# Kernel tuning notes

Hardware: AMD Instinct MI355X
Metric: run time of the kernel (lower is better)

The kernel has to match this reference:

```python
import jax, jax.numpy as jnp
import numpy as np

B, C, H = 8, 768, 12
TH = TW = 16
SH = SW = 32
N = TH * TW + SH * SW  # 1280


def setup_inputs() -> dict:
    key = jax.random.key(0)
    k1, k2, k3 = jax.random.split(key, 3)
    return {
        "x": jax.random.normal(k1, (B, N, C), jnp.float32),
        "qkv_w": jax.random.normal(k2, (3 * C, C), jnp.float32) * 0.02,
        "proj_w": jax.random.normal(k3, (C, C), jnp.float32) * 0.02,
        "proj_b": jnp.zeros((C,), jnp.float32),
        "t_h": TH, "t_w": TW, "s_h": SH, "s_w": SW,
    }


def reference(x, qkv_w, proj_w, proj_b, t_h, t_w, s_h, s_w):
    Bb, Nn, Cc = x.shape
    hd = Cc // H
    scale = hd ** -0.5
    nt = t_h * t_w
    ns = s_h * s_w
    # qkv projection: torch Linear computes x @ W.T
    qkv = (x @ qkv_w.T).reshape(Bb, Nn, 3, H, hd).transpose(2, 0, 3, 1, 4)
    q, k, v = qkv[0], qkv[1], qkv[2]  # each [B, H, N, hd]
    q_mt, q_s = q[:, :, :nt], q[:, :, nt:]
    k_mt, v_mt = k[:, :, :nt], v[:, :, :nt]
    # template queries attend only to template keys
    attn_t = jax.nn.softmax(jnp.einsum('bhqd,bhkd->bhqk', q_mt, k_mt) * scale, axis=-1)
    x_mt = jnp.einsum('bhqk,bhkd->bhqd', attn_t, v_mt).transpose(0, 2, 1, 3).reshape(Bb, nt, Cc)
    # search queries attend to all (template + search) keys
    attn_s = jax.nn.softmax(jnp.einsum('bhqd,bhkd->bhqk', q_s, k) * scale, axis=-1)
    x_s = jnp.einsum('bhqk,bhkd->bhqd', attn_s, v).transpose(0, 2, 1, 3).reshape(Bb, ns, Cc)
    out = jnp.concatenate([x_mt, x_s], axis=1)
    out = out @ proj_w.T + proj_b
    return out
```

## Files before the change

kernel.cpp:

```cpp
#include <hip/hip_runtime.h>
#include <hip/hip_bf16.h>


typedef __attribute__((ext_vector_type(8))) short s8v;
typedef __attribute__((ext_vector_type(4))) float f4v;
typedef __attribute__((ext_vector_type(4))) unsigned short u4v;
typedef __attribute__((ext_vector_type(4))) unsigned int u4i;
typedef __attribute__((ext_vector_type(2))) unsigned int u2i;

#define MFMA16(a, b, c) __builtin_amdgcn_mfma_f32_16x16x32_bf16((a), (b), (c), 0, 0, 0)

#define QSCALE 0.1803368801f

__device__ __forceinline__ unsigned short f2bf(float f) {
  unsigned int u = __builtin_bit_cast(unsigned int, f);
  u += 0x7fffu + ((u >> 16) & 1u);
  return (unsigned short)(u >> 16);
}

__device__ __forceinline__ unsigned int pk2(float lo, float hi) {
  __hip_bfloat162 t = __float22bfloat162_rn(make_float2(lo, hi));
  unsigned int u;
  __builtin_memcpy(&u, &t, 4);
  return u;
}

__device__ __forceinline__ s8v pack8(const float* p0, const float* p1) {
  u4i pi;
  pi[0] = pk2(p0[0], p0[1]);
  pi[1] = pk2(p0[2], p0[3]);
  pi[2] = pk2(p1[0], p1[1]);
  pi[3] = pk2(p1[2], p1[3]);
  return __builtin_bit_cast(s8v, pi);
}

__global__ __launch_bounds__(256) void cvt3_kernel(const float* __restrict__ x,
                                                   const float* __restrict__ wq,
                                                   const float* __restrict__ wp,
                                                   unsigned short* __restrict__ xb,
                                                   unsigned short* __restrict__ wqb,
                                                   unsigned short* __restrict__ wpb) {
  int i = blockIdx.x * 256 + threadIdx.x;
  const float* src;
  unsigned short* dst;
  int j;
  if (i < 1966080) {
    src = x; dst = xb; j = i;
  } else if (i < 1966080 + 442368) {
    src = wq; dst = wqb; j = i - 1966080;
  } else {
    src = wp; dst = wpb; j = i - (1966080 + 442368);
  }
  f4v v = ((const f4v*)src)[j];
  u4v o;
  o[0] = f2bf(v[0]); o[1] = f2bf(v[1]); o[2] = f2bf(v[2]); o[3] = f2bf(v[3]);
  ((u4v*)dst)[j] = o;
}


#define GEMM_STAGE(AS, BS, kt_)                                                             \
  do {                                                                                      \
    __builtin_amdgcn_global_load_lds(                                                       \
        (const __attribute__((address_space(1))) unsigned int*)(gA0 + (kt_)),               \
        (__attribute__((address_space(3))) unsigned int*)((char*)(AS) + tid * 16), 16, 0, 0); \
    __builtin_amdgcn_global_load_lds(                                                       \
        (const __attribute__((address_space(1))) unsigned int*)(gB0 + (kt_)),               \
        (__attribute__((address_space(3))) unsigned int*)((char*)(BS) + tid * 16), 16, 0, 0); \
    __builtin_amdgcn_global_load_lds(                                                       \
        (const __attribute__((address_space(1))) unsigned int*)(gA1 + (kt_)),               \
        (__attribute__((address_space(3))) unsigned int*)((char*)(AS) + (256 + tid) * 16),  \
        16, 0, 0);                                                                          \
    __builtin_amdgcn_global_load_lds(                                                       \
        (const __attribute__((address_space(1))) unsigned int*)(gB1 + (kt_)),               \
        (__attribute__((address_space(3))) unsigned int*)((char*)(BS) + (256 + tid) * 16),  \
        16, 0, 0);                                                                          \
  } while (0)

#define PIPE_WAIT4(cond_more)                                                               \
  do {                                                                                      \
    if (cond_more) asm volatile("s_waitcnt vmcnt(4) lgkmcnt(0)" ::: "memory");              \
    else           asm volatile("s_waitcnt vmcnt(0) lgkmcnt(0)" ::: "memory");              \
    __builtin_amdgcn_s_barrier();                                                           \
    __builtin_amdgcn_sched_barrier(0);                                                      \
  } while (0)

__global__ __launch_bounds__(256) void gemm_qkv_kernel(
    const unsigned short* __restrict__ A,
    const unsigned short* __restrict__ Bm,
    unsigned short* __restrict__ qb, unsigned short* __restrict__ kb,
    unsigned short* __restrict__ vT) {
  const int K = 768;
  __shared__ __align__(16) unsigned short As[3][128 * 32];
  __shared__ __align__(16) unsigned short Bs[3][128 * 32];
  int tid = threadIdx.x;
  int wave = tid >> 6, lane = tid & 63;
  int quad = lane >> 4, l16 = lane & 15;
  int wm = wave >> 1, wn = wave & 1;
  int l = blockIdx.x;
  int xcd = l & 7;
  int idx = l >> 3;
  int by = xcd * 10 + idx / 18;
  int bxg = idx - (idx / 18) * 18;
  int m0 = by * 128, n0 = bxg * 128;

  int srow = tid >> 2;
  int scol = (((tid & 3) ^ ((tid >> 3) & 3)) << 3);
  const unsigned short* gA0 = A + (size_t)(m0 + srow) * K + scol;
  const unsigned short* gA1 = A + (size_t)(m0 + srow + 64) * K + scol;
  const unsigned short* gB0 = Bm + (size_t)(n0 + srow) * K + scol;
  const unsigned short* gB1 = Bm + (size_t)(n0 + srow + 64) * K + scol;

  int rquad = quad ^ ((l16 >> 1) & 3);

  f4v acc[4][4];
#pragma unroll
  for (int i = 0; i < 4; ++i)
#pragma unroll
    for (int j = 0; j < 4; ++j) acc[i][j] = (f4v){0.f, 0.f, 0.f, 0.f};

  GEMM_STAGE(As[0], Bs[0], 0);
  GEMM_STAGE(As[1], Bs[1], 32);

  int bfc = 0, bfs = 2;
  for (int t = 0; t < 24; ++t) {
    PIPE_WAIT4(t + 1 < 24);
    if (t + 2 < 24) GEMM_STAGE(As[bfs], Bs[bfs], (t + 2) * 32);

    const unsigned short* Ab = As[bfc];
    const unsigned short* Bb = Bs[bfc];
    s8v af[4], bfr[4];
#pragma unroll
    for (int mi = 0; mi < 4; ++mi)
      af[mi] = *(const s8v*)&Ab[(wm * 64 + mi * 16 + l16) * 32 + rquad * 8];
#pragma unroll
    for (int ni = 0; ni < 4; ++ni)
      bfr[ni] = *(const s8v*)&Bb[(wn * 64 + ni * 16 + l16) * 32 + rquad * 8];
#pragma unroll
    for (int mi = 0; mi < 4; ++mi)
#pragma unroll
      for (int ni = 0; ni < 4; ++ni)
        acc[mi][ni] = MFMA16(af[mi], bfr[ni], acc[mi][ni]);

    bfc = (bfc == 2) ? 0 : bfc + 1;
    bfs = (bfs == 2) ? 0 : bfs + 1;
  }

  int which = n0 / 768;
  if (which == 2) {
#pragma unroll
    for (int ni = 0; ni < 4; ++ni) {
      int oo = n0 + wn * 64 + ni * 16 + l16 - 1536;
      int hh = oo >> 6;
      int dd = oo & 63;
#pragma unroll
      for (int mi = 0; mi < 4; ++mi) {
        int gm = m0 + wm * 64 + mi * 16 + quad * 4;
        int bb = gm / 1280;
        int nn = gm - bb * 1280;
        u2i w;
        w[0] = pk2(acc[mi][ni][0], acc[mi][ni][1]);
        w[1] = pk2(acc[mi][ni][2], acc[mi][ni][3]);
        *(u2i*)(vT + (((size_t)bb * 12 + hh) * 64 + dd) * 1280 + nn) = w;
      }
    }
  } else {
    unsigned short* dst = which ? kb : qb;
    float sc = which ? 1.0f : QSCALE;
#pragma unroll
    for (int ni = 0; ni < 4; ++ni) {
      int oo = n0 + wn * 64 + ni * 16 + l16 - which * 768;
      int hh = oo >> 6;
      int dd = oo & 63;
#pragma unroll
      for (int mi = 0; mi < 4; ++mi) {
#pragma unroll
        for (int r = 0; r < 4; ++r) {
          int gm = m0 + wm * 64 + mi * 16 + quad * 4 + r;
          int bb = gm / 1280;
          int nn = gm - bb * 1280;
          dst[(((size_t)bb * 12 + hh) * 1280 + nn) * 64 + dd] = f2bf(acc[mi][ni][r] * sc);
        }
      }
    }
  }
}

__global__ __launch_bounds__(256) void gemm_proj_kernel(
    const unsigned short* __restrict__ A,
    const unsigned short* __restrict__ Bm,
    const float* __restrict__ pb, float* __restrict__ out) {
  const int K = 768;
  __shared__ __align__(16) unsigned short As[3][128 * 32];
  __shared__ __align__(16) unsigned short Bs[3][128 * 32];
  int tid = threadIdx.x;
  int wave = tid >> 6, lane = tid & 63;
  int quad = lane >> 4, l16 = lane & 15;
  int wm = wave >> 1, wn = wave & 1;
  int l = blockIdx.x;
  int xcd = l & 7;
  int idx = l >> 3;
  int by = xcd * 10 + idx / 6;
  int bxg = idx - (idx / 6) * 6;
  int m0 = by * 128, n0 = bxg * 128;

  int srow = tid >> 2;
  int scol = (((tid & 3) ^ ((tid >> 3) & 3)) << 3);
  const unsigned short* gA0 = A + (size_t)(m0 + srow) * K + scol;
  const unsigned short* gA1 = A + (size_t)(m0 + srow + 64) * K + scol;
  const unsigned short* gB0 = Bm + (size_t)(n0 + srow) * K + scol;
  const unsigned short* gB1 = Bm + (size_t)(n0 + srow + 64) * K + scol;

  int rquad = quad ^ ((l16 >> 1) & 3);

  f4v acc[4][4];
#pragma unroll
  for (int i = 0; i < 4; ++i)
#pragma unroll
    for (int j = 0; j < 4; ++j) acc[i][j] = (f4v){0.f, 0.f, 0.f, 0.f};

  GEMM_STAGE(As[0], Bs[0], 0);
  GEMM_STAGE(As[1], Bs[1], 32);

  int bfc = 0, bfs = 2;
  for (int t = 0; t < 24; ++t) {
    PIPE_WAIT4(t + 1 < 24);
    if (t + 2 < 24) GEMM_STAGE(As[bfs], Bs[bfs], (t + 2) * 32);

    const unsigned short* Ab = As[bfc];
    const unsigned short* Bb = Bs[bfc];
    s8v af[4], bfr[4];
#pragma unroll
    for (int mi = 0; mi < 4; ++mi)
      af[mi] = *(const s8v*)&Ab[(wm * 64 + mi * 16 + l16) * 32 + rquad * 8];
#pragma unroll
    for (int ni = 0; ni < 4; ++ni)
      bfr[ni] = *(const s8v*)&Bb[(wn * 64 + ni * 16 + l16) * 32 + rquad * 8];
#pragma unroll
    for (int mi = 0; mi < 4; ++mi)
#pragma unroll
      for (int ni = 0; ni < 4; ++ni)
        acc[mi][ni] = MFMA16(af[mi], bfr[ni], acc[mi][ni]);

    bfc = (bfc == 2) ? 0 : bfc + 1;
    bfs = (bfs == 2) ? 0 : bfs + 1;
  }

#pragma unroll
  for (int ni = 0; ni < 4; ++ni) {
    int gn = n0 + wn * 64 + ni * 16 + l16;
    float bias = pb[gn];
#pragma unroll
    for (int mi = 0; mi < 4; ++mi)
#pragma unroll
      for (int r = 0; r < 4; ++r) {
        int gm = m0 + wm * 64 + mi * 16 + quad * 4 + r;
        out[(size_t)gm * 768 + gn] = acc[mi][ni][r] + bias;
      }
  }
}

__global__ __launch_bounds__(256) void attn_kernel(
    const unsigned short* __restrict__ qb, const unsigned short* __restrict__ kb,
    const unsigned short* __restrict__ vT, unsigned short* __restrict__ attnb) {
  const int NT = 1280, CC = 768;
  int l = blockIdx.x;
  int xcd = l & 7;
  int idx = l >> 3;
  int grp = xcd * 12 + idx / 10;
  int bx = idx - (idx / 10) * 10;
  int b = grp / 12;
  int h = grp - b * 12;
  int nk, qstart;
  if (bx < 8) { nk = 1280; qstart = 256 + bx * 128; }
  else        { nk = 256;  qstart = (bx - 8) * 128; }
  int wave = threadIdx.x >> 6, lane = threadIdx.x & 63;
  int quad = lane >> 4, l16 = lane & 15;
  int qa = qstart + wave * 32;
  int ntiles = nk >> 6;

  const unsigned short* qp = qb + (((size_t)b * 12 + h) * NT + qa) * 64;
  const unsigned short* kp = kb + (((size_t)b * 12 + h) * NT) * 64;
  const unsigned short* vp = vT + (((size_t)b * 12 + h) * 64) * NT;

  __shared__ __align__(16) unsigned short Kl[3][8][512];
  __shared__ __align__(16) unsigned short Vl[3][8][512];

  s8v bq0 = *(const s8v*)(qp + l16 * 64 + quad * 8);
  s8v bq1 = *(const s8v*)(qp + l16 * 64 + 32 + quad * 8);
  s8v bq2 = *(const s8v*)(qp + (16 + l16) * 64 + quad * 8);
  s8v bq3 = *(const s8v*)(qp + (16 + l16) * 64 + 32 + quad * 8);

  int perm = ((l16 >> 2) << 3) + (l16 & 3);
  int f0 = wave * 2, f1 = wave * 2 + 1;
  int koffs0, koffs1, voffs0, voffs1;
  {
    int s = f0 >> 2, dh = (f0 >> 1) & 1, hh = f0 & 1;
    koffs0 = (s * 32 + hh * 4 + perm) * 64 + (dh * 4 + quad) * 8;
    s = f1 >> 2; dh = (f1 >> 1) & 1; hh = f1 & 1;
    koffs1 = (s * 32 + hh * 4 + perm) * 64 + (dh * 4 + quad) * 8;
    int dt = f0 >> 1, sv = f0 & 1;
    voffs0 = (dt * 16 + l16) * NT + sv * 32 + quad * 8;
    dt = f1 >> 1; sv = f1 & 1;
    voffs1 = (dt * 16 + l16) * NT + sv * 32 + quad * 8;
  }

#define STAGE(bfi, k0_)                                                                     \
  do {                                                                                      \
    __builtin_amdgcn_global_load_lds(                                                       \
        (const __attribute__((address_space(1))) unsigned int*)(kp + (size_t)(k0_)*64 +     \
                                                                koffs0),                    \
        (__attribute__((address_space(3))) unsigned int*)((char*)&Kl[bfi][f0][0] +          \
                                                          lane * 16),                       \
        16, 0, 0);                                                                          \
    __builtin_amdgcn_global_load_lds(                                                       \
        (const __attribute__((address_space(1))) unsigned int*)(kp + (size_t)(k0_)*64 +     \
                                                                koffs1),                    \
        (__attribute__((address_space(3))) unsigned int*)((char*)&Kl[bfi][f1][0] +          \
                                                          lane * 16),                       \
        16, 0, 0);                                                                          \
    __builtin_amdgcn_global_load_lds(                                                       \
        (const __attribute__((address_space(1))) unsigned int*)(vp + (size_t)(k0_) +        \
                                                                voffs0),                    \
        (__attribute__((address_space(3))) unsigned int*)((char*)&Vl[bfi][f0][0] +          \
                                                          lane * 16),                       \
        16, 0, 0);                                                                          \
    __builtin_amdgcn_global_load_lds(                                                       \
        (const __attribute__((address_space(1))) unsigned int*)(vp + (size_t)(k0_) +        \
                                                                voffs1),                    \
        (__attribute__((address_space(3))) unsigned int*)((char*)&Vl[bfi][f1][0] +          \
                                                          lane * 16),                       \
        16, 0, 0);                                                                          \
  } while (0)

  float la = 0.f, lb = 0.f;
  f4v Oa[4], Ob[4];
#pragma unroll
  for (int dt = 0; dt < 4; ++dt) {
    Oa[dt] = (f4v){0.f, 0.f, 0.f, 0.f};
    Ob[dt] = (f4v){0.f, 0.f, 0.f, 0.f};
  }

  STAGE(0, 0);
  STAGE(1, 64);

  int bfc = 0, bfs = 2;
  for (int t = 0; t < ntiles; ++t) {
    PIPE_WAIT4(t + 1 < ntiles);
    if (t + 2 < ntiles) STAGE(bfs, (t + 2) * 64);

    s8v kf[8];
#pragma unroll
    for (int ff = 0; ff < 8; ++ff) kf[ff] = *(const s8v*)&Kl[bfc][ff][lane * 8];

#pragma unroll
    for (int s = 0; s < 2; ++s) {
      int s4 = s << 2;
      f4v s0a = {0.f, 0.f, 0.f, 0.f}, s1a = {0.f, 0.f, 0.f, 0.f};
      f4v s0b = {0.f, 0.f, 0.f, 0.f}, s1b = {0.f, 0.f, 0.f, 0.f};
      s0a = MFMA16(kf[s4 | 0], bq0, s0a);
      s0a = MFMA16(kf[s4 | 2], bq1, s0a);
      s1a = MFMA16(kf[s4 | 1], bq0, s1a);
      s1a = MFMA16(kf[s4 | 3], bq1, s1a);
      s0b = MFMA16(kf[s4 | 0], bq2, s0b);
      s0b = MFMA16(kf[s4 | 2], bq3, s0b);
      s1b = MFMA16(kf[s4 | 1], bq2, s1b);
      s1b = MFMA16(kf[s4 | 3], bq3, s1b);

      float p0a[4], p1a[4], p0b[4], p1b[4];
#pragma unroll
      for (int r = 0; r < 4; ++r) {
        p0a[r] = __builtin_amdgcn_exp2f(s0a[r]);
        p1a[r] = __builtin_amdgcn_exp2f(s1a[r]);
        p0b[r] = __builtin_amdgcn_exp2f(s0b[r]);
        p1b[r] = __builtin_amdgcn_exp2f(s1b[r]);
      }
      la += ((p0a[0] + p0a[1]) + (p0a[2] + p0a[3])) + ((p1a[0] + p1a[1]) + (p1a[2] + p1a[3]));
      lb += ((p0b[0] + p0b[1]) + (p0b[2] + p0b[3])) + ((p1b[0] + p1b[1]) + (p1b[2] + p1b[3]));

      s8v pa = pack8(p0a, p1a);
      s8v pbv = pack8(p0b, p1b);

      s8v vf[4];
#pragma unroll
      for (int dt = 0; dt < 4; ++dt) vf[dt] = *(const s8v*)&Vl[bfc][dt * 2 + s][lane * 8];
#pragma unroll
      for (int dt = 0; dt < 4; ++dt) {
        Oa[dt] = MFMA16(vf[dt], pa, Oa[dt]);
        Ob[dt] = MFMA16(vf[dt], pbv, Ob[dt]);
      }
    }

    bfc = (bfc == 2) ? 0 : bfc + 1;
    bfs = (bfs == 2) ? 0 : bfs + 1;
  }
#undef STAGE

  la += __shfl_xor(la, 16, 64);
  la += __shfl_xor(la, 32, 64);
  lb += __shfl_xor(lb, 16, 64);
  lb += __shfl_xor(lb, 32, 64);
  float inva = 1.f / la, invb = 1.f / lb;

  size_t rowa = ((size_t)b * NT + qa + l16) * CC + h * 64;
  size_t rowb = ((size_t)b * NT + qa + 16 + l16) * CC + h * 64;
#pragma unroll
  for (int dt = 0; dt < 4; ++dt) {
    u4v ova, ovb;
#pragma unroll
    for (int r = 0; r < 4; ++r) {
      ova[r] = f2bf(Oa[dt][r] * inva);
      ovb[r] = f2bf(Ob[dt][r] * invb);
    }
    *(u4v*)(attnb + rowa + dt * 16 + quad * 4) = ova;
    *(u4v*)(attnb + rowb + dt * 16 + quad * 4) = ovb;
  }
}

extern "C" void kernel_launch(void* const* d_in, const int* in_sizes, int n_in,
                              void* d_out, int out_size, void* d_ws, size_t ws_size,
                              hipStream_t stream) {
  const float* x = (const float*)d_in[0];
  const float* qkv_w = (const float*)d_in[1];
  const float* proj_w = (const float*)d_in[2];
  const float* proj_b = (const float*)d_in[3];
  float* out = (float*)d_out;

  char* ws = (char*)d_ws;
  unsigned short* xb = (unsigned short*)(ws + 0);
  unsigned short* wqkvb = (unsigned short*)(ws + 15728640);
  unsigned short* wpb = (unsigned short*)(ws + 19267584);
  unsigned short* qb = (unsigned short*)(ws + 20447232);
  unsigned short* kbuf = (unsigned short*)(ws + 36175872);
  unsigned short* vT = (unsigned short*)(ws + 51904512);
  unsigned short* attnb = xb;

  cvt3_kernel<<<dim3(9984), 256, 0, stream>>>(x, qkv_w, proj_w, xb, wqkvb, wpb);

  gemm_qkv_kernel<<<dim3(1440), 256, 0, stream>>>(xb, wqkvb, qb, kbuf, vT);
  attn_kernel<<<dim3(960), 256, 0, stream>>>(qb, kbuf, vT, attnb);
  gemm_proj_kernel<<<dim3(480), 256, 0, stream>>>(attnb, wpb, proj_b, out);
}
```

Baseline: 246.2 us.

## Double per-wave query rows in attention to reuse K/V tiles across 64 queries

Each wave now processes 64 query rows instead of 32, so every block covers 256 queries and the attention grid halves from 960 to 480 blocks. Each K/V tile staged in LDS and loaded into registers is reused for twice as many queries, reducing LDS traffic and global K/V loads per query. The cost is more accumulator registers per thread (four O sets), which may lower occupancy. Fewer blocks may also underfill the 256 CUs and worsen load balance between the long search blocks and the short template blocks.

```diff
diff --git a/kernel.cpp b/kernel.cpp
--- a/kernel.cpp
+++ b/kernel.cpp
@@ -266,16 +266,16 @@
   int l = blockIdx.x;
   int xcd = l & 7;
   int idx = l >> 3;
-  int grp = xcd * 12 + idx / 10;
-  int bx = idx - (idx / 10) * 10;
+  int grp = xcd * 12 + idx / 5;
+  int bx = idx - (idx / 5) * 5;
   int b = grp / 12;
   int h = grp - b * 12;
   int nk, qstart;
-  if (bx < 8) { nk = 1280; qstart = 256 + bx * 128; }
-  else        { nk = 256;  qstart = (bx - 8) * 128; }
+  if (bx < 4) { nk = 1280; qstart = 256 + bx * 256; }
+  else        { nk = 256;  qstart = 0; }
   int wave = threadIdx.x >> 6, lane = threadIdx.x & 63;
   int quad = lane >> 4, l16 = lane & 15;
-  int qa = qstart + wave * 32;
+  int qa = qstart + wave * 64;
   int ntiles = nk >> 6;
 
   const unsigned short* qp = qb + (((size_t)b * 12 + h) * NT + qa) * 64;
@@ -289,6 +289,10 @@
   s8v bq1 = *(const s8v*)(qp + l16 * 64 + 32 + quad * 8);
   s8v bq2 = *(const s8v*)(qp + (16 + l16) * 64 + quad * 8);
   s8v bq3 = *(const s8v*)(qp + (16 + l16) * 64 + 32 + quad * 8);
+  s8v bq4 = *(const s8v*)(qp + (32 + l16) * 64 + quad * 8);
+  s8v bq5 = *(const s8v*)(qp + (32 + l16) * 64 + 32 + quad * 8);
+  s8v bq6 = *(const s8v*)(qp + (48 + l16) * 64 + quad * 8);
+  s8v bq7 = *(const s8v*)(qp + (48 + l16) * 64 + 32 + quad * 8);
 
   int perm = ((l16 >> 2) << 3) + (l16 & 3);
   int f0 = wave * 2, f1 = wave * 2 + 1;
@@ -332,12 +336,45 @@
         16, 0, 0);                                                                          \
   } while (0)
 
-  float la = 0.f, lb = 0.f;
-  f4v Oa[4], Ob[4];
+#define GROUP(bqA, bqB, bqC, bqD, lA, lB, OA, OB)                                           \
+  do {                                                                                      \
+    f4v s0a = {0.f, 0.f, 0.f, 0.f}, s1a = {0.f, 0.f, 0.f, 0.f};                             \
+    f4v s0b = {0.f, 0.f, 0.f, 0.f}, s1b = {0.f, 0.f, 0.f, 0.f};                             \
+    s0a = MFMA16(kf[s4 | 0], bqA, s0a);                                                     \
+    s0a = MFMA16(kf[s4 | 2], bqB, s0a);                                                     \
+    s1a = MFMA16(kf[s4 | 1], bqA, s1a);                                                     \
+    s1a = MFMA16(kf[s4 | 3], bqB, s1a);                                                     \
+    s0b = MFMA16(kf[s4 | 0], bqC, s0b);                                                     \
+    s0b = MFMA16(kf[s4 | 2], bqD, s0b);                                                     \
+    s1b = MFMA16(kf[s4 | 1], bqC, s1b);                                                     \
+    s1b = MFMA16(kf[s4 | 3], bqD, s1b);                                                     \
+    float p0a[4], p1a[4], p0b[4], p1b[4];                                                   \
+    _Pragma("unroll") for (int r = 0; r < 4; ++r) {                                         \
+      p0a[r] = __builtin_amdgcn_exp2f(s0a[r]);                                              \
+      p1a[r] = __builtin_amdgcn_exp2f(s1a[r]);                                              \
+      p0b[r] = __builtin_amdgcn_exp2f(s0b[r]);                                              \
+      p1b[r] = __builtin_amdgcn_exp2f(s1b[r]);                                              \
+    }                                                                                       \
+    lA += ((p0a[0] + p0a[1]) + (p0a[2] + p0a[3])) +                                         \
+          ((p1a[0] + p1a[1]) + (p1a[2] + p1a[3]));                                          \
+    lB += ((p0b[0] + p0b[1]) + (p0b[2] + p0b[3])) +                                         \
+          ((p1b[0] + p1b[1]) + (p1b[2] + p1b[3]));                                          \
+    s8v pa = pack8(p0a, p1a);                                                               \
+    s8v pbv = pack8(p0b, p1b);                                                              \
+    _Pragma("unroll") for (int dt = 0; dt < 4; ++dt) {                                      \
+      OA[dt] = MFMA16(vf[dt], pa, OA[dt]);                                                  \
+      OB[dt] = MFMA16(vf[dt], pbv, OB[dt]);                                                 \
+    }                                                                                       \
+  } while (0)
+
+  float la = 0.f, lb = 0.f, lc = 0.f, ld = 0.f;
+  f4v Oa[4], Ob[4], Oc[4], Od[4];
 #pragma unroll
   for (int dt = 0; dt < 4; ++dt) {
     Oa[dt] = (f4v){0.f, 0.f, 0.f, 0.f};
     Ob[dt] = (f4v){0.f, 0.f, 0.f, 0.f};
+    Oc[dt] = (f4v){0.f, 0.f, 0.f, 0.f};
+    Od[dt] = (f4v){0.f, 0.f, 0.f, 0.f};
   }
 
   STAGE(0, 0);
@@ -355,64 +392,47 @@
 #pragma unroll
     for (int s = 0; s < 2; ++s) {
       int s4 = s << 2;
-      f4v s0a = {0.f, 0.f, 0.f, 0.f}, s1a = {0.f, 0.f, 0.f, 0.f};
-      f4v s0b = {0.f, 0.f, 0.f, 0.f}, s1b = {0.f, 0.f, 0.f, 0.f};
-      s0a = MFMA16(kf[s4 | 0], bq0, s0a);
-      s0a = MFMA16(kf[s4 | 2], bq1, s0a);
-      s1a = MFMA16(kf[s4 | 1], bq0, s1a);
-      s1a = MFMA16(kf[s4 | 3], bq1, s1a);
-      s0b = MFMA16(kf[s4 | 0], bq2, s0b);
-      s0b = MFMA16(kf[s4 | 2], bq3, s0b);
-      s1b = MFMA16(kf[s4 | 1], bq2, s1b);
-      s1b = MFMA16(kf[s4 | 3], bq3, s1b);
-
-      float p0a[4], p1a[4], p0b[4], p1b[4];
-#pragma unroll
-      for (int r = 0; r < 4; ++r) {
-        p0a[r] = __builtin_amdgcn_exp2f(s0a[r]);
-        p1a[r] = __builtin_amdgcn_exp2f(s1a[r]);
-        p0b[r] = __builtin_amdgcn_exp2f(s0b[r]);
-        p1b[r] = __builtin_amdgcn_exp2f(s1b[r]);
-      }
-      la += ((p0a[0] + p0a[1]) + (p0a[2] + p0a[3])) + ((p1a[0] + p1a[1]) + (p1a[2] + p1a[3]));
-      lb += ((p0b[0] + p0b[1]) + (p0b[2] + p0b[3])) + ((p1b[0] + p1b[1]) + (p1b[2] + p1b[3]));
-
-      s8v pa = pack8(p0a, p1a);
-      s8v pbv = pack8(p0b, p1b);
-
       s8v vf[4];
 #pragma unroll
       for (int dt = 0; dt < 4; ++dt) vf[dt] = *(const s8v*)&Vl[bfc][dt * 2 + s][lane * 8];
-#pragma unroll
-      for (int dt = 0; dt < 4; ++dt) {
-        Oa[dt] = MFMA16(vf[dt], pa, Oa[dt]);
-        Ob[dt] = MFMA16(vf[dt], pbv, Ob[dt]);
-      }
+      GROUP(bq0, bq1, bq2, bq3, la, lb, Oa, Ob);
+      GROUP(bq4, bq5, bq6, bq7, lc, ld, Oc, Od);
     }
 
     bfc = (bfc == 2) ? 0 : bfc + 1;
     bfs = (bfs == 2) ? 0 : bfs + 1;
   }
 #undef STAGE
+#undef GROUP
 
   la += __shfl_xor(la, 16, 64);
   la += __shfl_xor(la, 32, 64);
   lb += __shfl_xor(lb, 16, 64);
   lb += __shfl_xor(lb, 32, 64);
-  float inva = 1.f / la, invb = 1.f / lb;
+  lc += __shfl_xor(lc, 16, 64);
+  lc += __shfl_xor(lc, 32, 64);
+  ld += __shfl_xor(ld, 16, 64);
+  ld += __shfl_xor(ld, 32, 64);
+  float inva = 1.f / la, invb = 1.f / lb, invc = 1.f / lc, invd = 1.f / ld;
 
   size_t rowa = ((size_t)b * NT + qa + l16) * CC + h * 64;
   size_t rowb = ((size_t)b * NT + qa + 16 + l16) * CC + h * 64;
+  size_t rowc = ((size_t)b * NT + qa + 32 + l16) * CC + h * 64;
+  size_t rowd = ((size_t)b * NT + qa + 48 + l16) * CC + h * 64;
 #pragma unroll
   for (int dt = 0; dt < 4; ++dt) {
-    u4v ova, ovb;
+    u4v ova, ovb, ovc, ovd;
 #pragma unroll
     for (int r = 0; r < 4; ++r) {
       ova[r] = f2bf(Oa[dt][r] * inva);
       ovb[r] = f2bf(Ob[dt][r] * invb);
+      ovc[r] = f2bf(Oc[dt][r] * invc);
+      ovd[r] = f2bf(Od[dt][r] * invd);
     }
     *(u4v*)(attnb + rowa + dt * 16 + quad * 4) = ova;
     *(u4v*)(attnb + rowb + dt * 16 + quad * 4) = ovb;
+    *(u4v*)(attnb + rowc + dt * 16 + quad * 4) = ovc;
+    *(u4v*)(attnb + rowd + dt * 16 + quad * 4) = ovd;
   }
 }
 
@@ -437,6 +457,6 @@
   cvt3_kernel<<<dim3(9984), 256, 0, stream>>>(x, qkv_w, proj_w, xb, wqkvb, wpb);
 
   gemm_qkv_kernel<<<dim3(1440), 256, 0, stream>>>(xb, wqkvb, qb, kbuf, vT);
-  attn_kernel<<<dim3(960), 256, 0, stream>>>(qb, kbuf, vT, attnb);
+  attn_kernel<<<dim3(480), 256, 0, stream>>>(qb, kbuf, vT, attnb);
   gemm_proj_kernel<<<dim3(480), 256, 0, stream>>>(attnb, wpb, proj_b, out);
 }
```

After: 238.9 us. -3.0%, faster.
